# Performance work log

Measured on AMD Instinct MI355X. Metric: run time of the kernel, lower is better.

Reference implementation:

```python
import jax, jax.numpy as jnp
import numpy as np

B, N, M, E, H = 8, 4096, 4, 512, 8
HEAD_DIM = E // H
LN_EPS = 1e-5


def setup_inputs() -> dict:
    key = jax.random.key(0)
    ks = jax.random.split(key, 12)
    inp = {}
    for i in range(M):
        inp[f"f{i}"] = jax.random.normal(ks[i], (B, N, E), dtype=jnp.float32)
    # learned query (flattened from [1,1,E])
    inp["q_param"] = jax.random.normal(ks[4], (E,), dtype=jnp.float32)
    # torch nn.MultiheadAttention packed in-projection [3E, E] and bias [3E]
    inp["in_proj_w"] = jax.random.normal(ks[5], (3 * E, E), dtype=jnp.float32) * 0.02
    inp["in_proj_b"] = jnp.zeros((3 * E,), dtype=jnp.float32)
    inp["out_proj_w"] = jax.random.normal(ks[6], (E, E), dtype=jnp.float32) * 0.02
    inp["out_proj_b"] = jnp.zeros((E,), dtype=jnp.float32)
    inp["ln_gamma"] = jnp.ones((E,), dtype=jnp.float32)
    inp["ln_beta"] = jnp.zeros((E,), dtype=jnp.float32)
    return inp


def reference(f0, f1, f2, f3, q_param, in_proj_w, in_proj_b, out_proj_w, out_proj_b, ln_gamma, ln_beta):
    x = jnp.stack([f0, f1, f2, f3], axis=2)  # [B, N, M, E]
    b, n, m, e = x.shape
    h, d = H, e // H
    scale = 1.0 / np.sqrt(d)

    Wq, Wk, Wv = jnp.split(in_proj_w, 3, axis=0)  # each [E, E]
    bq, bk, bv = jnp.split(in_proj_b, 3)

    # single learned query, shared across all (b, n) instances
    qh = ((Wq @ q_param + bq) * scale).reshape(h, d)  # [H, d]

    k = (jnp.einsum('bnme,fe->bnmf', x, Wk) + bk).reshape(b, n, m, h, d)
    v = (jnp.einsum('bnme,fe->bnmf', x, Wv) + bv).reshape(b, n, m, h, d)

    scores = jnp.einsum('hd,bnmhd->bnhm', qh, k)        # [B, N, H, M]
    attn = jax.nn.softmax(scores, axis=-1)
    o = jnp.einsum('bnhm,bnmhd->bnhd', attn, v).reshape(b, n, e)
    o = o @ out_proj_w.T + out_proj_b                   # [B, N, E]

    mu = jnp.mean(o, axis=-1, keepdims=True)
    var = jnp.var(o, axis=-1, keepdims=True)
    return (o - mu) * jax.lax.rsqrt(var + LN_EPS) * ln_gamma + ln_beta
```

## Files before the change

kernel.cpp:

```cpp
#include <hip/hip_runtime.h>
#include <hip/hip_bf16.h>


typedef float  f32x4  __attribute__((ext_vector_type(4)));
typedef float  f32x16 __attribute__((ext_vector_type(16)));
typedef short  short8 __attribute__((ext_vector_type(8)));
typedef unsigned int u32x2 __attribute__((ext_vector_type(2)));

__device__ __forceinline__ unsigned short f2bf(float f) {
  unsigned int x = __float_as_uint(f);
  unsigned int r = (x + 0x7fffu + ((x >> 16) & 1u)) >> 16;
  return (unsigned short)r;
}

__device__ __forceinline__ short8 pack8(const f32x4& a, const f32x4& b) {
  unsigned int r0, r1, r2, r3;
  asm("v_cvt_pk_bf16_f32 %0, %1, %2" : "=v"(r0) : "v"(a[0]), "v"(a[1]));
  asm("v_cvt_pk_bf16_f32 %0, %1, %2" : "=v"(r1) : "v"(a[2]), "v"(a[3]));
  asm("v_cvt_pk_bf16_f32 %0, %1, %2" : "=v"(r2) : "v"(b[0]), "v"(b[1]));
  asm("v_cvt_pk_bf16_f32 %0, %1, %2" : "=v"(r3) : "v"(b[2]), "v"(b[3]));
  short8 r;
  r[0] = (short)(r0 & 0xffff); r[1] = (short)(r0 >> 16);
  r[2] = (short)(r1 & 0xffff); r[3] = (short)(r1 >> 16);
  r[4] = (short)(r2 & 0xffff); r[5] = (short)(r2 >> 16);
  r[6] = (short)(r3 & 0xffff); r[7] = (short)(r3 >> 16);
  return r;
}

__device__ __forceinline__ u32x2 pack4(const f32x4& a) {
  u32x2 r;
  asm("v_cvt_pk_bf16_f32 %0, %1, %2" : "=v"(r[0]) : "v"(a[0]), "v"(a[1]));
  asm("v_cvt_pk_bf16_f32 %0, %1, %2" : "=v"(r[1]) : "v"(a[2]), "v"(a[3]));
  return r;
}

__device__ __forceinline__ void mfma32(f32x16& c, short8 a, short8 b) {
  asm("v_mfma_f32_32x32x16_bf16 %0, %1, %2, %0" : "+v"(c) : "v"(a), "v"(b));
}
__device__ __forceinline__ void mfma16(f32x4& c, short8 a, short8 b) {
  asm("v_mfma_f32_16x16x32_bf16 %0, %1, %2, %0" : "+v"(c) : "v"(a), "v"(b));
}

__device__ __forceinline__ void gld4f(f32x4& d, const float* p) {
  asm volatile("global_load_dwordx4 %0, %1, off" : "=v"(d) : "v"(p));
}
__device__ __forceinline__ void gld4s(short8& d, const unsigned short* p) {
  asm volatile("global_load_dwordx4 %0, %1, off" : "=v"(d) : "v"(p));
}

__device__ __forceinline__ void wxv4(f32x4& a, f32x4& b, f32x4& c, f32x4& d) {
  asm volatile("s_waitcnt vmcnt(4)" : "+v"(a), "+v"(b), "+v"(c), "+v"(d));
}
__device__ __forceinline__ void wxv8(f32x4& a, f32x4& b, f32x4& c, f32x4& d) {
  asm volatile("s_waitcnt vmcnt(8)" : "+v"(a), "+v"(b), "+v"(c), "+v"(d));
}
__device__ __forceinline__ void wxv12(f32x4& a, f32x4& b, f32x4& c, f32x4& d) {
  asm volatile("s_waitcnt vmcnt(12)" : "+v"(a), "+v"(b), "+v"(c), "+v"(d));
}
__device__ __forceinline__ void wbv4(short8& a, short8& b, short8& c, short8& d,
                                     short8& e, short8& f, short8& g, short8& h) {
  asm volatile("s_waitcnt vmcnt(4)"
               : "+v"(a), "+v"(b), "+v"(c), "+v"(d),
                 "+v"(e), "+v"(f), "+v"(g), "+v"(h));
}
__device__ __forceinline__ void wbv0(short8& a, short8& b, short8& c, short8& d,
                                     short8& e, short8& f, short8& g, short8& h) {
  asm volatile("s_waitcnt vmcnt(0)"
               : "+v"(a), "+v"(b), "+v"(c), "+v"(d),
                 "+v"(e), "+v"(f), "+v"(g), "+v"(h));
}

__global__ void __launch_bounds__(512) tdcp_k0(
    const float* __restrict__ q_param, const float* __restrict__ in_w,
    const float* __restrict__ in_b, const float* __restrict__ out_w,
    float* __restrict__ scoreb, unsigned short* __restrict__ wscB,
    unsigned short* __restrict__ WvB, unsigned short* __restrict__ WoB)
{
  const int tid = threadIdx.x;
  const int blk = blockIdx.x;
  if (blk < 8) {
    const int h = blk;
    __shared__ float qls[512];
    __shared__ float qs[64];
    qls[tid] = q_param[tid];
    __syncthreads();
    {
      const int io = tid >> 3, sub = tid & 7;
      const float* wrow = in_w + (size_t)(h * 64 + io) * 512;
      float v = 0.f;
      #pragma unroll 8
      for (int ee = 0; ee < 64; ++ee) {
        const int e = sub + (ee << 3);
        v += wrow[e] * qls[e];
      }
      v += __shfl_xor(v, 1); v += __shfl_xor(v, 2); v += __shfl_xor(v, 4);
      if (sub == 0) qs[io] = (v + in_b[h * 64 + io]) * 0.125f;
    }
    __syncthreads();
    {
      const int e = tid;
      const float* wk = in_w + (size_t)(512 + h * 64) * 512 + e;
      float v = 0.f;
      #pragma unroll 8
      for (int jj = 0; jj < 64; ++jj) v += qs[jj] * wk[jj * 512];
      const int s32 = e >> 5, g = (e & 31) >> 3, j = e & 7;
      wscB[((s32 << 6) + h + (g << 4)) * 8 + j] = f2bf(v);
      wscB[((s32 << 6) + (h + 8) + (g << 4)) * 8 + j] = 0;
    }
    if (tid < 64) {
      float v = qs[tid] * in_b[512 + h * 64 + tid];
      v += __shfl_xor(v, 1);  v += __shfl_xor(v, 2);  v += __shfl_xor(v, 4);
      v += __shfl_xor(v, 8);  v += __shfl_xor(v, 16); v += __shfl_xor(v, 32);
      if (tid == 0) scoreb[h] = v;
    }
    if (blk == 0 && tid >= 64 && tid < 72) scoreb[tid - 56] = 0.f;
  } else {
    const int mb = blk - 8;
    const bool isWo = mb >= 64;
    const float* src = isWo ? out_w : (in_w + (size_t)1024 * 512);
    unsigned short* dst = isWo ? WoB : WvB;
    const int slot = ((mb & 63) << 9) + tid;
    const int ct = slot >> 11, kt = (slot >> 6) & 31, ln = slot & 63;
    const float* p = src + (size_t)(ct * 32 + (ln & 31)) * 512
                         + kt * 16 + ((ln >> 5) << 3);
    const f32x4 u0 = *(const f32x4*)(p);
    const f32x4 u1 = *(const f32x4*)(p + 4);
    short8 rr;
    rr[0] = (short)f2bf(u0[0]); rr[1] = (short)f2bf(u0[1]);
    rr[2] = (short)f2bf(u0[2]); rr[3] = (short)f2bf(u0[3]);
    rr[4] = (short)f2bf(u1[0]); rr[5] = (short)f2bf(u1[1]);
    rr[6] = (short)f2bf(u1[2]); rr[7] = (short)f2bf(u1[3]);
    *(short8*)(dst + slot * 8) = rr;
  }
}

__global__ void __launch_bounds__(512, 2) tdcp_k1(
    const float* __restrict__ f0, const float* __restrict__ f1,
    const float* __restrict__ f2, const float* __restrict__ f3,
    const float* __restrict__ in_b,
    const float* __restrict__ scoreb, const unsigned short* __restrict__ wscB,
    const unsigned short* __restrict__ WvB, const unsigned short* __restrict__ WoB,
    const float* __restrict__ out_b, const float* __restrict__ gamma,
    const float* __restrict__ beta, float* __restrict__ out)
{
  __shared__ __align__(16) char smem[65536];
  const int tid = threadIdx.x;
  const int w = tid >> 6;
  const int l = tid & 63;
  const int tok0 = blockIdx.x << 5;

  {
    const f32x4* wsrc = (const f32x4*)wscB;
    f32x4* wdst = (f32x4*)(smem + 49152);
    wdst[tid * 2] = wsrc[tid * 2];
    wdst[tid * 2 + 1] = wsrc[tid * 2 + 1];
  }

  const int sr = tid >> 2;
  const int c = tid & 3;
  const int sm = sr & 3;
  const int stk = sr >> 2;
  const float* fsrc = (sm == 0 ? f0 : sm == 1 ? f1 : sm == 2 ? f2 : f3)
                      + (size_t)(tok0 + stk) * 512 + (c << 2);
  int wj[4];
  #pragma unroll
  for (int j = 0; j < 4; ++j)
    wj[j] = (j << 12) + ((sr >> 5) << 10) + ((c >> 1) << 9)
          + ((((sr & 31) << 4)) ^ (j << 5)) + ((c & 1) << 3);

  const int aO = ((l >> 5) << 9) + ((l & 31) << 4);
  const int sBase = ((w >> 1) << 10) + (((l >> 4) & 1) << 9)
                  + ((((w & 1) << 4) | (l & 15)) << 4);
  const int ct0 = w << 1;
  const unsigned short* wv0 = WvB + (((ct0 * 32) << 6) + l) * 8;
  const unsigned short* wv1 = WvB + ((((ct0 + 1) * 32) << 6) + l) * 8;
  const unsigned short* wscL = (const unsigned short*)(smem + 49152);

  f32x16 acc[4][2];
  f32x4 sacc;
  #pragma unroll
  for (int i = 0; i < 4; ++i)
    #pragma unroll
    for (int cc = 0; cc < 2; ++cc)
      #pragma unroll
      for (int r = 0; r < 16; ++r) acc[i][cc][r] = 0.f;
  sacc[0] = sacc[1] = sacc[2] = sacc[3] = 0.f;

  f32x4 lx[2][4];
  short8 bb[2][8];

  gld4f(lx[0][0], fsrc);      gld4f(lx[0][1], fsrc + 16);
  gld4f(lx[0][2], fsrc + 32); gld4f(lx[0][3], fsrc + 48);
  gld4f(lx[1][0], fsrc + 64); gld4f(lx[1][1], fsrc + 80);
  gld4f(lx[1][2], fsrc + 96); gld4f(lx[1][3], fsrc + 112);
  wxv4(lx[0][0], lx[0][1], lx[0][2], lx[0][3]);
  #pragma unroll
  for (int j = 0; j < 4; ++j)
    *(u32x2*)(smem + wj[j]) = pack4(lx[0][j]);
  #pragma unroll
  for (int j = 0; j < 4; ++j) {
    gld4s(bb[0][2 * j],     wv0 + j * 512);
    gld4s(bb[0][2 * j + 1], wv1 + j * 512);
  }
  gld4f(lx[0][0], fsrc + 128); gld4f(lx[0][1], fsrc + 144);
  gld4f(lx[0][2], fsrc + 160); gld4f(lx[0][3], fsrc + 176);
  asm volatile("s_waitcnt lgkmcnt(0)" ::: "memory");
  __builtin_amdgcn_s_barrier();
  asm volatile("" ::: "memory");

  #pragma unroll
  for (int s = 0; s < 8; ++s) {
    if (s < 7) {
      f32x4 (&L)[4] = lx[(s + 1) & 1];
      if (s < 6) wxv12(L[0], L[1], L[2], L[3]);
      else       wxv8(L[0], L[1], L[2], L[3]);
      char* nb = smem + 16384 * ((s + 1) % 3);
      #pragma unroll
      for (int j = 0; j < 4; ++j)
        *(u32x2*)(nb + wj[j]) = pack4(L[j]);
    }
    asm volatile("s_waitcnt lgkmcnt(0)" ::: "memory");
    __builtin_amdgcn_s_barrier();
    asm volatile("" ::: "memory");

    short8 (&b)[8] = bb[s & 1];
    if (s < 6) wbv4(b[0], b[1], b[2], b[3], b[4], b[5], b[6], b[7]);
    else       wbv0(b[0], b[1], b[2], b[3], b[4], b[5], b[6], b[7]);
    char* cur = smem + 16384 * (s % 3);
    const short8 sb0 = *(const short8*)(wscL + (((2 * s) << 6) + l) * 8);
    const short8 sb1 = *(const short8*)(wscL + (((2 * s + 1) << 6) + l) * 8);
    #pragma unroll
    for (int kt4 = 0; kt4 < 4; ++kt4) {
      #pragma unroll
      for (int rt = 0; rt < 4; ++rt) {
        const short8 a = *(const short8*)(cur + (kt4 << 12) + (rt << 10)
                                          + (aO ^ (kt4 << 5)));
        mfma32(acc[rt][0], a, b[kt4 * 2]);
        mfma32(acc[rt][1], a, b[kt4 * 2 + 1]);
      }
      if ((kt4 & 1) == 0) {
        const int schunk = kt4 + (l >> 5);
        const short8 sa = *(const short8*)(cur + (schunk << 12)
                                           + (sBase ^ ((schunk & 3) << 5)));
        mfma16(sacc, sa, (kt4 == 0) ? sb0 : sb1);
      }
    }
    if (s < 7) {
      short8 (&nbf)[8] = bb[(s + 1) & 1];
      #pragma unroll
      for (int j = 0; j < 4; ++j) {
        gld4s(nbf[2 * j],     wv0 + ((s + 1) * 4 + j) * 512);
        gld4s(nbf[2 * j + 1], wv1 + ((s + 1) * 4 + j) * 512);
      }
    }
    if (s < 5) {
      f32x4 (&L)[4] = lx[(s + 3) & 1];
      const float* p = fsrc + ((s + 3) << 6);
      gld4f(L[0], p); gld4f(L[1], p + 16); gld4f(L[2], p + 32); gld4f(L[3], p + 48);
    }
  }
  asm volatile("s_nop 7\n\ts_nop 7\n\ts_nop 7" ::);

  {
    const int hh = l & 15;
    if (hh < 8) {
      const float sb = scoreb[hh];
      const float s0 = sacc[0] + sb, s1 = sacc[1] + sb;
      const float s2 = sacc[2] + sb, s3 = sacc[3] + sb;
      const float mx = fmaxf(fmaxf(s0, s1), fmaxf(s2, s3));
      const float e0 = __expf(s0 - mx), e1 = __expf(s1 - mx);
      const float e2 = __expf(s2 - mx), e3 = __expf(s3 - mx);
      const float inv = 1.f / (e0 + e1 + e2 + e3);
      f32x4 av; av[0] = e0 * inv; av[1] = e1 * inv; av[2] = e2 * inv; av[3] = e3 * inv;
      const int t = (w << 2) + (l >> 4);
      *(f32x4*)(smem + 32768 + (((t << 3) + hh) << 4)) = av;
    }
  }
  __syncthreads();

  {
    unsigned short* omid = (unsigned short*)(smem);
    #pragma unroll
    for (int c2 = 0; c2 < 2; ++c2) {
      const int ff = ((ct0 + c2) << 5) + (l & 31);
      const float bvf = in_b[1024 + ff];
      const int ktf = ff >> 4;
      const int laneL = ((l >> 3) & 1) << 5;
      const int elem = ff & 7;
      #pragma unroll
      for (int rt = 0; rt < 4; ++rt) {
        #pragma unroll
        for (int tt = 0; tt < 4; ++tt) {
          const int t = (rt << 3) + (tt << 1) + (l >> 5);
          const f32x4 av = *(const f32x4*)(smem + 32768 + (((t << 3) + w) << 4));
          const float o = av[0] * acc[rt][c2][tt * 4 + 0]
                        + av[1] * acc[rt][c2][tt * 4 + 1]
                        + av[2] * acc[rt][c2][tt * 4 + 2]
                        + av[3] * acc[rt][c2][tt * 4 + 3] + bvf;
          omid[((ktf << 6) + t + laneL) * 8 + elem] = f2bf(o);
        }
      }
    }
  }
  __syncthreads();

  f32x16 oa0, oa1;
  #pragma unroll
  for (int r = 0; r < 16; ++r) { oa0[r] = 0.f; oa1[r] = 0.f; }
  const unsigned short* wo0 = WoB + (((ct0 * 32) << 6) + l) * 8;
  const unsigned short* wo1 = WoB + ((((ct0 + 1) * 32) << 6) + l) * 8;
  const int a_off = l << 4;
  #pragma unroll 4
  for (int kt = 0; kt < 32; ++kt) {
    const short8 a = *(const short8*)(smem + (kt << 10) + a_off);
    mfma32(oa0, a, *(const short8*)(wo0 + kt * 512));
    mfma32(oa1, a, *(const short8*)(wo1 + kt * 512));
  }
  asm volatile("s_nop 7\n\ts_nop 7\n\ts_nop 7" ::);

  {
    const int g0 = (ct0 << 5) + (l & 31);
    const int g1 = g0 + 32;
    const float ob0 = out_b[g0], ob1 = out_b[g1];
    const float gm0 = gamma[g0], gm1 = gamma[g1];
    const float bt0 = beta[g0],  bt1 = beta[g1];
    float* stats = (float*)(smem + 36864);
    #pragma unroll
    for (int r = 0; r < 16; ++r) {
      const float v0 = oa0[r] + ob0, v1 = oa1[r] + ob1;
      float s = v0 + v1, qq = v0 * v0 + v1 * v1;
      s += __shfl_xor(s, 16); qq += __shfl_xor(qq, 16);
      s += __shfl_xor(s, 8);  qq += __shfl_xor(qq, 8);
      s += __shfl_xor(s, 4);  qq += __shfl_xor(qq, 4);
      s += __shfl_xor(s, 2);  qq += __shfl_xor(qq, 2);
      s += __shfl_xor(s, 1);  qq += __shfl_xor(qq, 1);
      if ((l & 31) == 0) {
        const int t = (r & 3) + ((r >> 2) << 3) + ((l >> 5) << 2);
        stats[(t << 4) + (w << 1)] = s;
        stats[(t << 4) + (w << 1) + 1] = qq;
      }
    }
    __syncthreads();
    #pragma unroll
    for (int r = 0; r < 16; ++r) {
      const int t = (r & 3) + ((r >> 2) << 3) + ((l >> 5) << 2);
      const float* st = stats + (t << 4);
      float s = 0.f, qq = 0.f;
      #pragma unroll
      for (int ww = 0; ww < 8; ++ww) { s += st[2 * ww]; qq += st[2 * ww + 1]; }
      const float mu = s * 0.001953125f;
      const float rs = rsqrtf(qq * 0.001953125f - mu * mu + 1e-5f);
      const float v0 = oa0[r] + ob0, v1 = oa1[r] + ob1;
      float* op = out + (size_t)(tok0 + t) * 512;
      op[g0] = (v0 - mu) * rs * gm0 + bt0;
      op[g1] = (v1 - mu) * rs * gm1 + bt1;
    }
  }
}

extern "C" void kernel_launch(void* const* d_in, const int* in_sizes, int n_in,
                              void* d_out, int out_size, void* d_ws, size_t ws_size,
                              hipStream_t stream) {
  const float* f0      = (const float*)d_in[0];
  const float* f1      = (const float*)d_in[1];
  const float* f2      = (const float*)d_in[2];
  const float* f3      = (const float*)d_in[3];
  const float* q_param = (const float*)d_in[4];
  const float* in_w    = (const float*)d_in[5];
  const float* in_b    = (const float*)d_in[6];
  const float* out_w   = (const float*)d_in[7];
  const float* out_b   = (const float*)d_in[8];
  const float* gamma   = (const float*)d_in[9];
  const float* beta    = (const float*)d_in[10];
  float* out = (float*)d_out;

  char* ws = (char*)d_ws;
  float* scoreb          = (float*)ws;
  unsigned short* wscB   = (unsigned short*)(ws + 4096);
  unsigned short* WvB    = (unsigned short*)(ws + 20480);
  unsigned short* WoB    = (unsigned short*)(ws + 544768);

  tdcp_k0<<<136, 512, 0, stream>>>(q_param, in_w, in_b, out_w,
                                   scoreb, wscB, WvB, WoB);
  tdcp_k1<<<1024, 512, 0, stream>>>(f0, f1, f2, f3, in_b,
                                    scoreb, wscB, WvB, WoB,
                                    out_b, gamma, beta, out);
}
```

Measured before the change: 149.0 us.

## Restructure K/V projection pipeline to process two stages per barrier with 4 LDS buffers

Replaces the 8-step triple-buffered loop with a hand-unrolled schedule that packs two input stages into a 4-slot LDS ring and computes two stages between each barrier. This halves the number of workgroup barriers and deepens the global-load prefetch, with higher vmcnt thresholds. LDS grows to 80 KB of dynamic shared memory, set via hipFuncSetAttribute. That could lower occupancy from 2 blocks per CU and raises register pressure from more in-flight loads. An extra __syncthreads is added before the softmax stage, which reuses the LDS region.

```diff
diff --git a/kernel.cpp b/kernel.cpp
--- a/kernel.cpp
+++ b/kernel.cpp
@@ -11,20 +11,6 @@
   unsigned int x = __float_as_uint(f);
   unsigned int r = (x + 0x7fffu + ((x >> 16) & 1u)) >> 16;
   return (unsigned short)r;
-}
-
-__device__ __forceinline__ short8 pack8(const f32x4& a, const f32x4& b) {
-  unsigned int r0, r1, r2, r3;
-  asm("v_cvt_pk_bf16_f32 %0, %1, %2" : "=v"(r0) : "v"(a[0]), "v"(a[1]));
-  asm("v_cvt_pk_bf16_f32 %0, %1, %2" : "=v"(r1) : "v"(a[2]), "v"(a[3]));
-  asm("v_cvt_pk_bf16_f32 %0, %1, %2" : "=v"(r2) : "v"(b[0]), "v"(b[1]));
-  asm("v_cvt_pk_bf16_f32 %0, %1, %2" : "=v"(r3) : "v"(b[2]), "v"(b[3]));
-  short8 r;
-  r[0] = (short)(r0 & 0xffff); r[1] = (short)(r0 >> 16);
-  r[2] = (short)(r1 & 0xffff); r[3] = (short)(r1 >> 16);
-  r[4] = (short)(r2 & 0xffff); r[5] = (short)(r2 >> 16);
-  r[6] = (short)(r3 & 0xffff); r[7] = (short)(r3 >> 16);
-  return r;
 }
 
 __device__ __forceinline__ u32x2 pack4(const f32x4& a) {
@@ -51,15 +37,21 @@
 __device__ __forceinline__ void wxv4(f32x4& a, f32x4& b, f32x4& c, f32x4& d) {
   asm volatile("s_waitcnt vmcnt(4)" : "+v"(a), "+v"(b), "+v"(c), "+v"(d));
 }
-__device__ __forceinline__ void wxv8(f32x4& a, f32x4& b, f32x4& c, f32x4& d) {
-  asm volatile("s_waitcnt vmcnt(8)" : "+v"(a), "+v"(b), "+v"(c), "+v"(d));
-}
-__device__ __forceinline__ void wxv12(f32x4& a, f32x4& b, f32x4& c, f32x4& d) {
-  asm volatile("s_waitcnt vmcnt(12)" : "+v"(a), "+v"(b), "+v"(c), "+v"(d));
-}
-__device__ __forceinline__ void wbv4(short8& a, short8& b, short8& c, short8& d,
+__device__ __forceinline__ void wlx16(f32x4& a, f32x4& b, f32x4& c, f32x4& d,
+                                      f32x4& e, f32x4& f, f32x4& g, f32x4& h) {
+  asm volatile("s_waitcnt vmcnt(16)"
+               : "+v"(a), "+v"(b), "+v"(c), "+v"(d),
+                 "+v"(e), "+v"(f), "+v"(g), "+v"(h));
+}
+__device__ __forceinline__ void wbv16(short8& a, short8& b, short8& c, short8& d,
+                                      short8& e, short8& f, short8& g, short8& h) {
+  asm volatile("s_waitcnt vmcnt(16)"
+               : "+v"(a), "+v"(b), "+v"(c), "+v"(d),
+                 "+v"(e), "+v"(f), "+v"(g), "+v"(h));
+}
+__device__ __forceinline__ void wbv8(short8& a, short8& b, short8& c, short8& d,
                                      short8& e, short8& f, short8& g, short8& h) {
-  asm volatile("s_waitcnt vmcnt(4)"
+  asm volatile("s_waitcnt vmcnt(8)"
                : "+v"(a), "+v"(b), "+v"(c), "+v"(d),
                  "+v"(e), "+v"(f), "+v"(g), "+v"(h));
 }
@@ -143,7 +135,7 @@
     const float* __restrict__ out_b, const float* __restrict__ gamma,
     const float* __restrict__ beta, float* __restrict__ out)
 {
-  __shared__ __align__(16) char smem[65536];
+  extern __shared__ __align__(16) char smem[];
   const int tid = threadIdx.x;
   const int w = tid >> 6;
   const int l = tid & 63;
@@ -151,7 +143,7 @@
 
   {
     const f32x4* wsrc = (const f32x4*)wscB;
-    f32x4* wdst = (f32x4*)(smem + 49152);
+    f32x4* wdst = (f32x4*)(smem + 65536);
     wdst[tid * 2] = wsrc[tid * 2];
     wdst[tid * 2 + 1] = wsrc[tid * 2 + 1];
   }
@@ -174,7 +166,7 @@
   const int ct0 = w << 1;
   const unsigned short* wv0 = WvB + (((ct0 * 32) << 6) + l) * 8;
   const unsigned short* wv1 = WvB + ((((ct0 + 1) * 32) << 6) + l) * 8;
-  const unsigned short* wscL = (const unsigned short*)(smem + 49152);
+  const unsigned short* wscL = (const unsigned short*)(smem + 65536);
 
   f32x16 acc[4][2];
   f32x4 sacc;
@@ -189,77 +181,118 @@
   f32x4 lx[2][4];
   short8 bb[2][8];
 
-  gld4f(lx[0][0], fsrc);      gld4f(lx[0][1], fsrc + 16);
-  gld4f(lx[0][2], fsrc + 32); gld4f(lx[0][3], fsrc + 48);
-  gld4f(lx[1][0], fsrc + 64); gld4f(lx[1][1], fsrc + 80);
-  gld4f(lx[1][2], fsrc + 96); gld4f(lx[1][3], fsrc + 112);
+#define PACKSTEP(sc, bank) do {                                   \
+    char* nb_ = smem + (((sc) & 3) << 14);                        \
+    *(u32x2*)(nb_ + wj[0]) = pack4(lx[bank][0]);                  \
+    *(u32x2*)(nb_ + wj[1]) = pack4(lx[bank][1]);                  \
+    *(u32x2*)(nb_ + wj[2]) = pack4(lx[bank][2]);                  \
+    *(u32x2*)(nb_ + wj[3]) = pack4(lx[bank][3]);                  \
+  } while (0)
+
+#define ISSUE_L(sc, bank) do {                                    \
+    const float* p_ = fsrc + ((sc) << 6);                         \
+    gld4f(lx[bank][0], p_);      gld4f(lx[bank][1], p_ + 16);     \
+    gld4f(lx[bank][2], p_ + 32); gld4f(lx[bank][3], p_ + 48);     \
+  } while (0)
+
+#define ISSUE_B(sc, bank) do {                                    \
+    gld4s(bb[bank][0], wv0 + ((sc) * 4 + 0) * 512);               \
+    gld4s(bb[bank][1], wv1 + ((sc) * 4 + 0) * 512);               \
+    gld4s(bb[bank][2], wv0 + ((sc) * 4 + 1) * 512);               \
+    gld4s(bb[bank][3], wv1 + ((sc) * 4 + 1) * 512);               \
+    gld4s(bb[bank][4], wv0 + ((sc) * 4 + 2) * 512);               \
+    gld4s(bb[bank][5], wv1 + ((sc) * 4 + 2) * 512);               \
+    gld4s(bb[bank][6], wv0 + ((sc) * 4 + 3) * 512);               \
+    gld4s(bb[bank][7], wv1 + ((sc) * 4 + 3) * 512);               \
+  } while (0)
+
+#define COMPUTE(sc, bank) do {                                              \
+    char* cur_ = smem + (((sc) & 3) << 14);                                 \
+    const short8 sb0_ = *(const short8*)(wscL + (((2*(sc)) << 6) + l) * 8); \
+    const short8 sb1_ = *(const short8*)(wscL + (((2*(sc)+1) << 6) + l) * 8);\
+    __builtin_amdgcn_s_setprio(1);                                          \
+    _Pragma("unroll")                                                       \
+    for (int kt4 = 0; kt4 < 4; ++kt4) {                                     \
+      _Pragma("unroll")                                                     \
+      for (int rt = 0; rt < 4; ++rt) {                                      \
+        const short8 a_ = *(const short8*)(cur_ + (kt4 << 12) + (rt << 10)  \
+                                           + (aO ^ (kt4 << 5)));            \
+        mfma32(acc[rt][0], a_, bb[bank][kt4 * 2]);                          \
+        mfma32(acc[rt][1], a_, bb[bank][kt4 * 2 + 1]);                      \
+      }                                                                     \
+      if ((kt4 & 1) == 0) {                                                 \
+        const int schunk_ = kt4 + (l >> 5);                                 \
+        const short8 sa_ = *(const short8*)(cur_ + (schunk_ << 12)          \
+                                            + (sBase ^ ((schunk_ & 3) << 5)));\
+        mfma16(sacc, sa_, (kt4 == 0) ? sb0_ : sb1_);                        \
+      }                                                                     \
+    }                                                                       \
+    __builtin_amdgcn_s_setprio(0);                                          \
+  } while (0)
+
+#define WPACK() wlx16(lx[0][0], lx[0][1], lx[0][2], lx[0][3],               \
+                      lx[1][0], lx[1][1], lx[1][2], lx[1][3])
+#define WB16(k) wbv16(bb[k][0], bb[k][1], bb[k][2], bb[k][3],               \
+                      bb[k][4], bb[k][5], bb[k][6], bb[k][7])
+#define WB8(k)  wbv8(bb[k][0], bb[k][1], bb[k][2], bb[k][3],                \
+                     bb[k][4], bb[k][5], bb[k][6], bb[k][7])
+#define WB0(k)  wbv0(bb[k][0], bb[k][1], bb[k][2], bb[k][3],                \
+                     bb[k][4], bb[k][5], bb[k][6], bb[k][7])
+#define BARRIER() do {                                            \
+    asm volatile("s_waitcnt lgkmcnt(0)" ::: "memory");            \
+    __builtin_amdgcn_s_barrier();                                 \
+    asm volatile("" ::: "memory");                                \
+  } while (0)
+
+  ISSUE_L(0, 0); ISSUE_L(1, 1);
   wxv4(lx[0][0], lx[0][1], lx[0][2], lx[0][3]);
-  #pragma unroll
-  for (int j = 0; j < 4; ++j)
-    *(u32x2*)(smem + wj[j]) = pack4(lx[0][j]);
-  #pragma unroll
-  for (int j = 0; j < 4; ++j) {
-    gld4s(bb[0][2 * j],     wv0 + j * 512);
-    gld4s(bb[0][2 * j + 1], wv1 + j * 512);
-  }
-  gld4f(lx[0][0], fsrc + 128); gld4f(lx[0][1], fsrc + 144);
-  gld4f(lx[0][2], fsrc + 160); gld4f(lx[0][3], fsrc + 176);
-  asm volatile("s_waitcnt lgkmcnt(0)" ::: "memory");
-  __builtin_amdgcn_s_barrier();
-  asm volatile("" ::: "memory");
-
-  #pragma unroll
-  for (int s = 0; s < 8; ++s) {
-    if (s < 7) {
-      f32x4 (&L)[4] = lx[(s + 1) & 1];
-      if (s < 6) wxv12(L[0], L[1], L[2], L[3]);
-      else       wxv8(L[0], L[1], L[2], L[3]);
-      char* nb = smem + 16384 * ((s + 1) % 3);
-      #pragma unroll
-      for (int j = 0; j < 4; ++j)
-        *(u32x2*)(nb + wj[j]) = pack4(L[j]);
-    }
-    asm volatile("s_waitcnt lgkmcnt(0)" ::: "memory");
-    __builtin_amdgcn_s_barrier();
-    asm volatile("" ::: "memory");
-
-    short8 (&b)[8] = bb[s & 1];
-    if (s < 6) wbv4(b[0], b[1], b[2], b[3], b[4], b[5], b[6], b[7]);
-    else       wbv0(b[0], b[1], b[2], b[3], b[4], b[5], b[6], b[7]);
-    char* cur = smem + 16384 * (s % 3);
-    const short8 sb0 = *(const short8*)(wscL + (((2 * s) << 6) + l) * 8);
-    const short8 sb1 = *(const short8*)(wscL + (((2 * s + 1) << 6) + l) * 8);
-    #pragma unroll
-    for (int kt4 = 0; kt4 < 4; ++kt4) {
-      #pragma unroll
-      for (int rt = 0; rt < 4; ++rt) {
-        const short8 a = *(const short8*)(cur + (kt4 << 12) + (rt << 10)
-                                          + (aO ^ (kt4 << 5)));
-        mfma32(acc[rt][0], a, b[kt4 * 2]);
-        mfma32(acc[rt][1], a, b[kt4 * 2 + 1]);
-      }
-      if ((kt4 & 1) == 0) {
-        const int schunk = kt4 + (l >> 5);
-        const short8 sa = *(const short8*)(cur + (schunk << 12)
-                                           + (sBase ^ ((schunk & 3) << 5)));
-        mfma16(sacc, sa, (kt4 == 0) ? sb0 : sb1);
-      }
-    }
-    if (s < 7) {
-      short8 (&nbf)[8] = bb[(s + 1) & 1];
-      #pragma unroll
-      for (int j = 0; j < 4; ++j) {
-        gld4s(nbf[2 * j],     wv0 + ((s + 1) * 4 + j) * 512);
-        gld4s(nbf[2 * j + 1], wv1 + ((s + 1) * 4 + j) * 512);
-      }
-    }
-    if (s < 5) {
-      f32x4 (&L)[4] = lx[(s + 3) & 1];
-      const float* p = fsrc + ((s + 3) << 6);
-      gld4f(L[0], p); gld4f(L[1], p + 16); gld4f(L[2], p + 32); gld4f(L[3], p + 48);
-    }
-  }
+  PACKSTEP(0, 0);
+  ISSUE_L(2, 0);
+  wxv4(lx[1][0], lx[1][1], lx[1][2], lx[1][3]);
+  PACKSTEP(1, 1);
+  ISSUE_L(3, 1);
+  ISSUE_B(0, 0); ISSUE_B(1, 1);
+
+  BARRIER();
+  WPACK();
+  PACKSTEP(2, 0); PACKSTEP(3, 1);
+  ISSUE_L(4, 0); ISSUE_L(5, 1);
+  WB16(0);
+  COMPUTE(0, 0);
+  ISSUE_B(2, 0);
+  WB16(1);
+  COMPUTE(1, 1);
+  ISSUE_B(3, 1);
+
+  BARRIER();
+  WPACK();
+  PACKSTEP(4, 0); PACKSTEP(5, 1);
+  ISSUE_L(6, 0); ISSUE_L(7, 1);
+  WB16(0);
+  COMPUTE(2, 0);
+  ISSUE_B(4, 0);
+  WB16(1);
+  COMPUTE(3, 1);
+  ISSUE_B(5, 1);
+
+  BARRIER();
+  WPACK();
+  PACKSTEP(6, 0); PACKSTEP(7, 1);
+  WB8(0);
+  COMPUTE(4, 0);
+  ISSUE_B(6, 0);
+  WB8(1);
+  COMPUTE(5, 1);
+  ISSUE_B(7, 1);
+
+  BARRIER();
+  WB8(0);
+  COMPUTE(6, 0);
+  WB0(1);
+  COMPUTE(7, 1);
+
   asm volatile("s_nop 7\n\ts_nop 7\n\ts_nop 7" ::);
+  __syncthreads();
 
   {
     const int hh = l & 15;
@@ -273,7 +306,7 @@
       const float inv = 1.f / (e0 + e1 + e2 + e3);
       f32x4 av; av[0] = e0 * inv; av[1] = e1 * inv; av[2] = e2 * inv; av[3] = e3 * inv;
       const int t = (w << 2) + (l >> 4);
-      *(f32x4*)(smem + 32768 + (((t << 3) + hh) << 4)) = av;
+      *(f32x4*)(smem + 65536 + (((t << 3) + hh) << 4)) = av;
     }
   }
   __syncthreads();
@@ -292,7 +325,7 @@
         #pragma unroll
         for (int tt = 0; tt < 4; ++tt) {
           const int t = (rt << 3) + (tt << 1) + (l >> 5);
-          const f32x4 av = *(const f32x4*)(smem + 32768 + (((t << 3) + w) << 4));
+          const f32x4 av = *(const f32x4*)(smem + 65536 + (((t << 3) + w) << 4));
           const float o = av[0] * acc[rt][c2][tt * 4 + 0]
                         + av[1] * acc[rt][c2][tt * 4 + 1]
                         + av[2] * acc[rt][c2][tt * 4 + 2]
@@ -324,7 +357,7 @@
     const float ob0 = out_b[g0], ob1 = out_b[g1];
     const float gm0 = gamma[g0], gm1 = gamma[g1];
     const float bt0 = beta[g0],  bt1 = beta[g1];
-    float* stats = (float*)(smem + 36864);
+    float* stats = (float*)(smem + 69632);
     #pragma unroll
     for (int r = 0; r < 16; ++r) {
       const float v0 = oa0[r] + ob0, v1 = oa1[r] + ob1;
@@ -356,6 +389,15 @@
       op[g1] = (v1 - mu) * rs * gm1 + bt1;
     }
   }
+#undef PACKSTEP
+#undef ISSUE_L
+#undef ISSUE_B
+#undef COMPUTE
+#undef WPACK
+#undef WB16
+#undef WB8
+#undef WB0
+#undef BARRIER
 }
 
 extern "C" void kernel_launch(void* const* d_in, const int* in_sizes, int n_in,
@@ -380,9 +422,12 @@
   unsigned short* WvB    = (unsigned short*)(ws + 20480);
   unsigned short* WoB    = (unsigned short*)(ws + 544768);
 
+  hipFuncSetAttribute((const void*)tdcp_k1,
+                      hipFuncAttributeMaxDynamicSharedMemorySize, 81920);
+
   tdcp_k0<<<136, 512, 0, stream>>>(q_param, in_w, in_b, out_w,
                                    scoreb, wscB, WvB, WoB);
-  tdcp_k1<<<1024, 512, 0, stream>>>(f0, f1, f2, f3, in_b,
-                                    scoreb, wscB, WvB, WoB,
-                                    out_b, gamma, beta, out);
-}
+  tdcp_k1<<<1024, 512, 81920, stream>>>(f0, f1, f2, f3, in_b,
+                                        scoreb, wscB, WvB, WoB,
+                                        out_b, gamma, beta, out);
+}
```

New measurement: 161.0 us. 1.08x slower.

## Stream fp32 features into LDS via direct global-to-LDS loads, convert to bf16 at read

Applied to the files above, without the earlier changes.

Replaces register-staged feature loads (global load, bf16 pack, LDS store) with global_load_lds DMA that writes raw fp32 tiles into a triple-buffered, XOR-swizzled LDS layout. Conversion to bf16 now happens after reading from LDS, just before the MFMAs, and the wait/barrier schedule is restructured around the new vmcnt accounting. The intent is to cut VGPR pressure and VALU/LDS-store work in the producer path. In exchange, LDS use grows to 112 KB per block, which limits occupancy to one block per CU despite launch_bounds(512,2), and the fp32 reads double LDS read traffic.

```diff
diff --git a/kernel.cpp b/kernel.cpp
--- a/kernel.cpp
+++ b/kernel.cpp
@@ -5,7 +5,9 @@
 typedef float  f32x4  __attribute__((ext_vector_type(4)));
 typedef float  f32x16 __attribute__((ext_vector_type(16)));
 typedef short  short8 __attribute__((ext_vector_type(8)));
-typedef unsigned int u32x2 __attribute__((ext_vector_type(2)));
+
+typedef __attribute__((address_space(1))) const void GV;
+typedef __attribute__((address_space(3))) void LV;
 
 __device__ __forceinline__ unsigned short f2bf(float f) {
   unsigned int x = __float_as_uint(f);
@@ -27,13 +29,6 @@
   return r;
 }
 
-__device__ __forceinline__ u32x2 pack4(const f32x4& a) {
-  u32x2 r;
-  asm("v_cvt_pk_bf16_f32 %0, %1, %2" : "=v"(r[0]) : "v"(a[0]), "v"(a[1]));
-  asm("v_cvt_pk_bf16_f32 %0, %1, %2" : "=v"(r[1]) : "v"(a[2]), "v"(a[3]));
-  return r;
-}
-
 __device__ __forceinline__ void mfma32(f32x16& c, short8 a, short8 b) {
   asm("v_mfma_f32_32x32x16_bf16 %0, %1, %2, %0" : "+v"(c) : "v"(a), "v"(b));
 }
@@ -41,25 +36,21 @@
   asm("v_mfma_f32_16x16x32_bf16 %0, %1, %2, %0" : "+v"(c) : "v"(a), "v"(b));
 }
 
-__device__ __forceinline__ void gld4f(f32x4& d, const float* p) {
-  asm volatile("global_load_dwordx4 %0, %1, off" : "=v"(d) : "v"(p));
-}
 __device__ __forceinline__ void gld4s(short8& d, const unsigned short* p) {
   asm volatile("global_load_dwordx4 %0, %1, off" : "=v"(d) : "v"(p));
 }
 
-__device__ __forceinline__ void wxv4(f32x4& a, f32x4& b, f32x4& c, f32x4& d) {
-  asm volatile("s_waitcnt vmcnt(4)" : "+v"(a), "+v"(b), "+v"(c), "+v"(d));
-}
-__device__ __forceinline__ void wxv8(f32x4& a, f32x4& b, f32x4& c, f32x4& d) {
-  asm volatile("s_waitcnt vmcnt(8)" : "+v"(a), "+v"(b), "+v"(c), "+v"(d));
-}
-__device__ __forceinline__ void wxv12(f32x4& a, f32x4& b, f32x4& c, f32x4& d) {
-  asm volatile("s_waitcnt vmcnt(12)" : "+v"(a), "+v"(b), "+v"(c), "+v"(d));
-}
-__device__ __forceinline__ void wbv4(short8& a, short8& b, short8& c, short8& d,
+#define WAITV(n) asm volatile("s_waitcnt vmcnt(" #n ")" ::: "memory")
+
+__device__ __forceinline__ void wbv12(short8& a, short8& b, short8& c, short8& d,
+                                      short8& e, short8& f, short8& g, short8& h) {
+  asm volatile("s_waitcnt vmcnt(12)"
+               : "+v"(a), "+v"(b), "+v"(c), "+v"(d),
+                 "+v"(e), "+v"(f), "+v"(g), "+v"(h));
+}
+__device__ __forceinline__ void wbv8(short8& a, short8& b, short8& c, short8& d,
                                      short8& e, short8& f, short8& g, short8& h) {
-  asm volatile("s_waitcnt vmcnt(4)"
+  asm volatile("s_waitcnt vmcnt(8)"
                : "+v"(a), "+v"(b), "+v"(c), "+v"(d),
                  "+v"(e), "+v"(f), "+v"(g), "+v"(h));
 }
@@ -143,7 +134,7 @@
     const float* __restrict__ out_b, const float* __restrict__ gamma,
     const float* __restrict__ beta, float* __restrict__ out)
 {
-  __shared__ __align__(16) char smem[65536];
+  extern __shared__ __align__(16) char smem[];
   const int tid = threadIdx.x;
   const int w = tid >> 6;
   const int l = tid & 63;
@@ -151,30 +142,37 @@
 
   {
     const f32x4* wsrc = (const f32x4*)wscB;
-    f32x4* wdst = (f32x4*)(smem + 49152);
+    f32x4* wdst = (f32x4*)(smem + 98304);
     wdst[tid * 2] = wsrc[tid * 2];
     wdst[tid * 2 + 1] = wsrc[tid * 2 + 1];
   }
 
-  const int sr = tid >> 2;
-  const int c = tid & 3;
-  const int sm = sr & 3;
-  const int stk = sr >> 2;
-  const float* fsrc = (sm == 0 ? f0 : sm == 1 ? f1 : sm == 2 ? f2 : f3)
-                      + (size_t)(tok0 + stk) * 512 + (c << 2);
-  int wj[4];
-  #pragma unroll
-  for (int j = 0; j < 4; ++j)
-    wj[j] = (j << 12) + ((sr >> 5) << 10) + ((c >> 1) << 9)
-          + ((((sr & 31) << 4)) ^ (j << 5)) + ((c & 1) << 3);
-
-  const int aO = ((l >> 5) << 9) + ((l & 31) << 4);
-  const int sBase = ((w >> 1) << 10) + (((l >> 4) & 1) << 9)
-                  + ((((w & 1) << 4) | (l & 15)) << 4);
+  const float* gsrc[4];
+  #pragma unroll
+  for (int q = 0; q < 4; ++q) {
+    const int R = 16 * w + 4 * q + (l >> 4);
+    const int m = R & 3, tok = R >> 2;
+    const int u = (((l & 15) >> 1) ^ (R & 7));
+    gsrc[q] = (m == 0 ? f0 : m == 1 ? f1 : m == 2 ? f2 : f3)
+              + (size_t)(tok0 + tok) * 512 + (u << 3) + ((l & 1) << 2);
+  }
+  const int dmaDst = (w << 12);
+
+  const int aB = (l & 31) << 8;
+  int offA[4];
+  #pragma unroll
+  for (int kt4 = 0; kt4 < 4; ++kt4)
+    offA[kt4] = (((2 * kt4 + (l >> 5)) ^ (l & 7)) << 5);
+  const int sB = (16 * w + (l & 15)) << 8;
+  int offS[2];
+  #pragma unroll
+  for (int sc = 0; sc < 2; ++sc)
+    offS[sc] = (((4 * sc + (l >> 4)) ^ (l & 7)) << 5);
+
   const int ct0 = w << 1;
   const unsigned short* wv0 = WvB + (((ct0 * 32) << 6) + l) * 8;
   const unsigned short* wv1 = WvB + ((((ct0 + 1) * 32) << 6) + l) * 8;
-  const unsigned short* wscL = (const unsigned short*)(smem + 49152);
+  const unsigned short* wscL = (const unsigned short*)(smem + 98304);
 
   f32x16 acc[4][2];
   f32x4 sacc;
@@ -186,77 +184,73 @@
       for (int r = 0; r < 16; ++r) acc[i][cc][r] = 0.f;
   sacc[0] = sacc[1] = sacc[2] = sacc[3] = 0.f;
 
-  f32x4 lx[2][4];
   short8 bb[2][8];
 
-  gld4f(lx[0][0], fsrc);      gld4f(lx[0][1], fsrc + 16);
-  gld4f(lx[0][2], fsrc + 32); gld4f(lx[0][3], fsrc + 48);
-  gld4f(lx[1][0], fsrc + 64); gld4f(lx[1][1], fsrc + 80);
-  gld4f(lx[1][2], fsrc + 96); gld4f(lx[1][3], fsrc + 112);
-  wxv4(lx[0][0], lx[0][1], lx[0][2], lx[0][3]);
-  #pragma unroll
-  for (int j = 0; j < 4; ++j)
-    *(u32x2*)(smem + wj[j]) = pack4(lx[0][j]);
-  #pragma unroll
-  for (int j = 0; j < 4; ++j) {
-    gld4s(bb[0][2 * j],     wv0 + j * 512);
-    gld4s(bb[0][2 * j + 1], wv1 + j * 512);
-  }
-  gld4f(lx[0][0], fsrc + 128); gld4f(lx[0][1], fsrc + 144);
-  gld4f(lx[0][2], fsrc + 160); gld4f(lx[0][3], fsrc + 176);
+#define DMA(S) do { \
+    char* db_ = smem + 32768 * ((S) % 3) + dmaDst; \
+    __builtin_amdgcn_global_load_lds((GV*)(gsrc[0] + (S) * 64), (LV*)(db_),        16, 0, 0); \
+    __builtin_amdgcn_global_load_lds((GV*)(gsrc[1] + (S) * 64), (LV*)(db_ + 1024), 16, 0, 0); \
+    __builtin_amdgcn_global_load_lds((GV*)(gsrc[2] + (S) * 64), (LV*)(db_ + 2048), 16, 0, 0); \
+    __builtin_amdgcn_global_load_lds((GV*)(gsrc[3] + (S) * 64), (LV*)(db_ + 3072), 16, 0, 0); \
+  } while (0)
+
+#define ISSUE_B(S, bank) do { \
+    gld4s(bb[bank][0], wv0 + ((S) * 4 + 0) * 512); \
+    gld4s(bb[bank][1], wv1 + ((S) * 4 + 0) * 512); \
+    gld4s(bb[bank][2], wv0 + ((S) * 4 + 1) * 512); \
+    gld4s(bb[bank][3], wv1 + ((S) * 4 + 1) * 512); \
+    gld4s(bb[bank][4], wv0 + ((S) * 4 + 2) * 512); \
+    gld4s(bb[bank][5], wv1 + ((S) * 4 + 2) * 512); \
+    gld4s(bb[bank][6], wv0 + ((S) * 4 + 3) * 512); \
+    gld4s(bb[bank][7], wv1 + ((S) * 4 + 3) * 512); \
+  } while (0)
+
+  DMA(0); DMA(1);
+  ISSUE_B(0, 0);
+  WAITV(12);
   asm volatile("s_waitcnt lgkmcnt(0)" ::: "memory");
   __builtin_amdgcn_s_barrier();
   asm volatile("" ::: "memory");
 
   #pragma unroll
   for (int s = 0; s < 8; ++s) {
-    if (s < 7) {
-      f32x4 (&L)[4] = lx[(s + 1) & 1];
-      if (s < 6) wxv12(L[0], L[1], L[2], L[3]);
-      else       wxv8(L[0], L[1], L[2], L[3]);
-      char* nb = smem + 16384 * ((s + 1) % 3);
-      #pragma unroll
-      for (int j = 0; j < 4; ++j)
-        *(u32x2*)(nb + wj[j]) = pack4(L[j]);
-    }
-    asm volatile("s_waitcnt lgkmcnt(0)" ::: "memory");
-    __builtin_amdgcn_s_barrier();
-    asm volatile("" ::: "memory");
+    if (s < 6) DMA(s + 2);
+    if (s < 7) ISSUE_B(s + 1, (s + 1) & 1);
 
     short8 (&b)[8] = bb[s & 1];
-    if (s < 6) wbv4(b[0], b[1], b[2], b[3], b[4], b[5], b[6], b[7]);
-    else       wbv0(b[0], b[1], b[2], b[3], b[4], b[5], b[6], b[7]);
-    char* cur = smem + 16384 * (s % 3);
+    if (s < 6)      wbv12(b[0], b[1], b[2], b[3], b[4], b[5], b[6], b[7]);
+    else if (s == 6) wbv8(b[0], b[1], b[2], b[3], b[4], b[5], b[6], b[7]);
+    else             wbv0(b[0], b[1], b[2], b[3], b[4], b[5], b[6], b[7]);
+
+    const char* cur = smem + 32768 * (s % 3);
     const short8 sb0 = *(const short8*)(wscL + (((2 * s) << 6) + l) * 8);
     const short8 sb1 = *(const short8*)(wscL + (((2 * s + 1) << 6) + l) * 8);
     #pragma unroll
     for (int kt4 = 0; kt4 < 4; ++kt4) {
       #pragma unroll
       for (int rt = 0; rt < 4; ++rt) {
-        const short8 a = *(const short8*)(cur + (kt4 << 12) + (rt << 10)
-                                          + (aO ^ (kt4 << 5)));
+        const char* p = cur + (rt << 13) + aB + offA[kt4];
+        const f32x4 lo = *(const f32x4*)(p);
+        const f32x4 hi = *(const f32x4*)(p + 16);
+        const short8 a = pack8(lo, hi);
         mfma32(acc[rt][0], a, b[kt4 * 2]);
         mfma32(acc[rt][1], a, b[kt4 * 2 + 1]);
       }
       if ((kt4 & 1) == 0) {
-        const int schunk = kt4 + (l >> 5);
-        const short8 sa = *(const short8*)(cur + (schunk << 12)
-                                           + (sBase ^ ((schunk & 3) << 5)));
-        mfma16(sacc, sa, (kt4 == 0) ? sb0 : sb1);
-      }
-    }
+        const int sc = kt4 >> 1;
+        const char* p = cur + sB + offS[sc];
+        const f32x4 lo = *(const f32x4*)(p);
+        const f32x4 hi = *(const f32x4*)(p + 16);
+        mfma16(sacc, pack8(lo, hi), (sc == 0) ? sb0 : sb1);
+      }
+    }
+
+    if (s < 6)      { WAITV(12); }
+    else if (s == 6) { WAITV(8); }
     if (s < 7) {
-      short8 (&nbf)[8] = bb[(s + 1) & 1];
-      #pragma unroll
-      for (int j = 0; j < 4; ++j) {
-        gld4s(nbf[2 * j],     wv0 + ((s + 1) * 4 + j) * 512);
-        gld4s(nbf[2 * j + 1], wv1 + ((s + 1) * 4 + j) * 512);
-      }
-    }
-    if (s < 5) {
-      f32x4 (&L)[4] = lx[(s + 3) & 1];
-      const float* p = fsrc + ((s + 3) << 6);
-      gld4f(L[0], p); gld4f(L[1], p + 16); gld4f(L[2], p + 32); gld4f(L[3], p + 48);
+      asm volatile("s_waitcnt lgkmcnt(0)" ::: "memory");
+      __builtin_amdgcn_s_barrier();
+      asm volatile("" ::: "memory");
     }
   }
   asm volatile("s_nop 7\n\ts_nop 7\n\ts_nop 7" ::);
@@ -273,7 +267,7 @@
       const float inv = 1.f / (e0 + e1 + e2 + e3);
       f32x4 av; av[0] = e0 * inv; av[1] = e1 * inv; av[2] = e2 * inv; av[3] = e3 * inv;
       const int t = (w << 2) + (l >> 4);
-      *(f32x4*)(smem + 32768 + (((t << 3) + hh) << 4)) = av;
+      *(f32x4*)(smem + 65536 + (((t << 3) + hh) << 4)) = av;
     }
   }
   __syncthreads();
@@ -292,7 +286,7 @@
         #pragma unroll
         for (int tt = 0; tt < 4; ++tt) {
           const int t = (rt << 3) + (tt << 1) + (l >> 5);
-          const f32x4 av = *(const f32x4*)(smem + 32768 + (((t << 3) + w) << 4));
+          const f32x4 av = *(const f32x4*)(smem + 65536 + (((t << 3) + w) << 4));
           const float o = av[0] * acc[rt][c2][tt * 4 + 0]
                         + av[1] * acc[rt][c2][tt * 4 + 1]
                         + av[2] * acc[rt][c2][tt * 4 + 2]
@@ -324,7 +318,7 @@
     const float ob0 = out_b[g0], ob1 = out_b[g1];
     const float gm0 = gamma[g0], gm1 = gamma[g1];
     const float bt0 = beta[g0],  bt1 = beta[g1];
-    float* stats = (float*)(smem + 36864);
+    float* stats = (float*)(smem + 69632);
     #pragma unroll
     for (int r = 0; r < 16; ++r) {
       const float v0 = oa0[r] + ob0, v1 = oa1[r] + ob1;
@@ -356,6 +350,8 @@
       op[g1] = (v1 - mu) * rs * gm1 + bt1;
     }
   }
+#undef DMA
+#undef ISSUE_B
 }
 
 extern "C" void kernel_launch(void* const* d_in, const int* in_sizes, int n_in,
@@ -380,9 +376,12 @@
   unsigned short* WvB    = (unsigned short*)(ws + 20480);
   unsigned short* WoB    = (unsigned short*)(ws + 544768);
 
+  hipFuncSetAttribute((const void*)tdcp_k1,
+                      hipFuncAttributeMaxDynamicSharedMemorySize, 114688);
+
   tdcp_k0<<<136, 512, 0, stream>>>(q_param, in_w, in_b, out_w,
                                    scoreb, wscB, WvB, WoB);
-  tdcp_k1<<<1024, 512, 0, stream>>>(f0, f1, f2, f3, in_b,
-                                    scoreb, wscB, WvB, WoB,
-                                    out_b, gamma, beta, out);
-}
+  tdcp_k1<<<1024, 512, 114688, stream>>>(f0, f1, f2, f3, in_b,
+                                         scoreb, wscB, WvB, WoB,
+                                         out_b, gamma, beta, out);
+}
```

After: 154.2 us. 3.5% more time.
